# Kernel tuning notes

Measured on AMD Instinct MI355X. Metric: run time of the kernel, lower is better.

The kernel has to match this reference:

```python
import jax, jax.numpy as jnp
import numpy as np

N, E, F, DIM, BT, RANK = 8192, 32768, 16, 64, 4, 512
EDGE_VARIABLE = 2


def setup_inputs() -> dict:
    key = jax.random.key(0)
    ks = jax.random.split(key, 24)

    def rn(i, shape, s=0.05):
        return jax.random.normal(ks[i], shape, dtype=jnp.float32) * s

    x = jax.random.normal(ks[0], (N, F), dtype=jnp.float32)
    # first feature column is a categorical node-type id (EDGE_VARIABLE == 2)
    x = x.at[:, 0].set(jax.random.randint(ks[1], (N,), 0, 5).astype(jnp.float32))
    edge_index = jax.random.randint(ks[2], (2, E), 0, N, dtype=jnp.int32)
    edge_attr = jax.random.uniform(ks[3], (E, BT), dtype=jnp.float32)
    return {
        'x': x, 'edge_index': edge_index, 'edge_attr': edge_attr,
        'W0': rn(4, (DIM, F)), 'b0': jnp.zeros(DIM, jnp.float32),
        'nnW1': rn(5, (32, BT)), 'nnb1': jnp.zeros(32, jnp.float32),
        'nnW2': rn(6, (DIM * DIM, 32), 0.02), 'nnb2': jnp.zeros(DIM * DIM, jnp.float32),
        'root': rn(7, (DIM, DIM)), 'conv_b': jnp.zeros(DIM, jnp.float32),
        'Wih': rn(8, (3 * DIM, DIM)), 'Whh': rn(9, (3 * DIM, DIM)),
        'bih': jnp.zeros(3 * DIM, jnp.float32), 'bhh': jnp.zeros(3 * DIM, jnp.float32),
        'W1l': rn(10, (BT, DIM)), 'b1l': jnp.zeros(BT, jnp.float32),
        'WUp': rn(11, (DIM, BT)), 'bUp': jnp.zeros(DIM, jnp.float32),
        'WDown': rn(12, (BT, DIM)), 'bDown': jnp.zeros(BT, jnp.float32),
        'U': rn(13, (BT, RANK, DIM)), 'V': rn(14, (BT, DIM, RANK)),
        'weight': rn(15, (1, DIM), 1.0), 'linW': rn(16, (DIM, DIM)), 'linb': jnp.zeros(DIM, jnp.float32),
        'weight_e': rn(17, (1, BT), 1.0), 'linWe': rn(18, (BT, BT)), 'linbe': jnp.zeros(BT, jnp.float32),
    }


def _gru_cell(m, h, Wih, Whh, bih, bhh):
    # torch GRU gate order: reset, update, new
    gi = m @ Wih.T + bih
    gh = h @ Whh.T + bhh
    ir, iz, i_n = jnp.split(gi, 3, axis=-1)
    hr, hz, h_n = jnp.split(gh, 3, axis=-1)
    r = jax.nn.sigmoid(ir + hr)
    z = jax.nn.sigmoid(iz + hz)
    n = jnp.tanh(i_n + r * h_n)
    return (1.0 - z) * n + z * h


def reference(x, edge_index, edge_attr,
              W0, b0, nnW1, nnb1, nnW2, nnb2, root, conv_b,
              Wih, Whh, bih, bhh, W1l, b1l, WUp, bUp, WDown, bDown,
              U, V, weight, linW, linb, weight_e, linWe, linbe):
    n_nodes = x.shape[0]
    src, dst = edge_index[0], edge_index[1]

    out = jax.nn.relu(x @ W0.T + b0)            # [N, DIM]
    h = out

    # mean-aggregation degree (clamped)
    deg = jnp.clip(jax.ops.segment_sum(jnp.ones_like(src, dtype=out.dtype), dst,
                                       num_segments=n_nodes), 1.0)[:, None]

    # edge-conditioned per-edge weight matrices  [E, DIM, DIM]
    We = (jax.nn.relu(edge_attr @ nnW1.T + nnb1) @ nnW2.T + nnb2).reshape(-1, DIM, DIM)

    for _ in range(3):  # 3 message-passing + GRU steps
        msg = jnp.einsum('ei,eio->eo', out[src], We)                 # per-edge matvec
        agg = jax.ops.segment_sum(msg, dst, num_segments=n_nodes) / deg
        m = jax.nn.relu(out @ root + agg + conv_b)                    # NNConv(root + mean msg)
        h = _gru_cell(m, h, Wih, Whh, bih, bhh)
        out = h

    out_edges = jax.nn.relu(out @ W1l.T + b1l)                        # [N, BT]

    # combine node state with upscaled edge-variable state
    ev_mask = (x[:, 0] == EDGE_VARIABLE)
    out_combine = jnp.where(ev_mask[:, None], out_edges @ WUp.T + bUp, out)

    # FGNet factorized (rank-512) bond-type-conditioned message passing
    bond = jnp.argmax(edge_attr, axis=-1)                             # [E]
    oh = jax.nn.one_hot(bond, BT, dtype=out.dtype)                    # [E, BT]
    h_src = out_combine[src]                                          # [E, DIM]
    zf = jnp.einsum('ed,tdr->etr', h_src, V)                          # [E, BT, RANK]
    zsel = jnp.einsum('etr,et->er', zf, oh)                           # select factor by bond type
    me = jnp.einsum('er,et,trd->ed', zsel, oh, U)                     # [E, DIM]
    msg_f = jax.nn.relu(jax.ops.segment_sum(me, dst, num_segments=n_nodes) / deg)
    msg_to_edge = msg_f @ WDown.T + bDown                             # [N, BT]

    out = out + jax.nn.relu((weight * msg_f) @ linW.T + linb)
    out_edges = out_edges + jax.nn.relu((weight_e * msg_to_edge) @ linWe.T + linbe)
    return jax.nn.log_softmax(out_edges, axis=-1)
```

## Files before the change

### kernel.cpp

```cpp
#include <hip/hip_runtime.h>
#include <hip/hip_bf16.h>

#define NN 8192
#define NE 32768
#define FD 16
#define DIM 64
#define BT 4
#define RANK 512

typedef __attribute__((ext_vector_type(8))) short bf16x8;
typedef __attribute__((ext_vector_type(4))) float f32x4;

__device__ inline unsigned short f2bf(float f) {
    union { float f; unsigned u; } c; c.f = f;
    return (unsigned short)((c.u + 0x7fffu + ((c.u >> 16) & 1u)) >> 16);
}
__device__ inline float ubf(unsigned short h) {
    union { unsigned u; float f; } c; c.u = ((unsigned)h) << 16; return c.f;
}
__device__ inline float bflo(unsigned u) { union { unsigned u; float f; } c; c.u = u << 16; return c.f; }
__device__ inline float bfhi(unsigned u) { union { unsigned u; float f; } c; c.u = u & 0xffff0000u; return c.f; }

__global__ __launch_bounds__(256) void k_prep(
    const float* __restrict__ x, const int* __restrict__ ei, const float* __restrict__ ea,
    const float* __restrict__ W0, const float* __restrict__ b0,
    const float* __restrict__ nnW1, const float* __restrict__ nnb1,
    const float* __restrict__ W2, const float* __restrict__ Wih, const float* __restrict__ Whh,
    const float* __restrict__ root, const float* __restrict__ b2,
    const float* __restrict__ U, const float* __restrict__ V,
    float* __restrict__ s, unsigned short* __restrict__ shi, unsigned short* __restrict__ slo,
    float* __restrict__ deg, int* __restrict__ srccnt,
    float* __restrict__ h32, int* __restrict__ bond,
    unsigned short* __restrict__ w2h, unsigned short* __restrict__ w2l,
    unsigned short* __restrict__ wihh, unsigned short* __restrict__ wihl,
    unsigned short* __restrict__ whhh, unsigned short* __restrict__ whhl,
    unsigned short* __restrict__ rth, unsigned short* __restrict__ rtl,
    unsigned short* __restrict__ b2th, unsigned short* __restrict__ b2tl,
    float* __restrict__ M)
{
    int bid = blockIdx.x, tid = threadIdx.x;
    if (bid < 2048) {
        int gid = bid * 256 + tid;
        int n = gid >> 6, d = gid & 63;
        const float4* xr = (const float4*)(x + (size_t)n * FD);
        const float4* wr = (const float4*)(W0 + d * FD);
        float4 x0 = xr[0], x1 = xr[1], x2 = xr[2], x3 = xr[3];
        float4 w0 = wr[0], w1 = wr[1], w2 = wr[2], w3 = wr[3];
        float acc = b0[d]
            + x0.x*w0.x + x0.y*w0.y + x0.z*w0.z + x0.w*w0.w
            + x1.x*w1.x + x1.y*w1.y + x1.z*w1.z + x1.w*w1.w
            + x2.x*w2.x + x2.y*w2.y + x2.z*w2.z + x2.w*w2.w
            + x3.x*w3.x + x3.y*w3.y + x3.z*w3.z + x3.w*w3.w;
        float sv = fmaxf(acc, 0.f);
        s[gid] = sv;
        unsigned short h = f2bf(sv);
        shi[gid] = h; slo[gid] = f2bf(sv - ubf(h));
    } else if (bid < 2176) {
        int e = (bid - 2048) * 256 + tid;
        atomicAdd(&deg[ei[NE + e]], 1.0f);
        atomicAdd(&srccnt[ei[e]], 1);
    } else if (bid < 6272) {
        int e = (bid - 2176) * 8 + (tid >> 5);
        int k = tid & 31;
        float a0 = ea[e * 4 + 0], a1 = ea[e * 4 + 1], a2 = ea[e * 4 + 2], a3 = ea[e * 4 + 3];
        float h = nnb1[k] + a0 * nnW1[k * 4 + 0] + a1 * nnW1[k * 4 + 1]
                          + a2 * nnW1[k * 4 + 2] + a3 * nnW1[k * 4 + 3];
        h32[e * 32 + k] = fmaxf(h, 0.f);
        if (k == 0) {
            int bi = 0; float bv = a0;
            if (a1 > bv) { bv = a1; bi = 1; }
            if (a2 > bv) { bv = a2; bi = 2; }
            if (a3 > bv) { bv = a3; bi = 3; }
            bond[e] = bi;
        }
    } else if (bid < 6784) {
        int gid = (bid - 6272) * 256 + tid;
        int col = gid >> 6, i = gid & 63;
        float v = W2[(size_t)(i * 64 + (col >> 5)) * 32 + (col & 31)];
        unsigned short h = f2bf(v);
        w2h[gid] = h; w2l[gid] = f2bf(v - ubf(h));
    } else if (bid < 6880) {
        int gid = (bid - 6784) * 256 + tid;
        if (gid < 12288) {
            float v = Wih[gid];
            unsigned short h = f2bf(v);
            wihh[gid] = h; wihl[gid] = f2bf(v - ubf(h));
        } else {
            int g = gid - 12288;
            float v = Whh[g];
            unsigned short h = f2bf(v);
            whhh[g] = h; whhl[g] = f2bf(v - ubf(h));
        }
    } else if (bid < 6896) {
        int gid = (bid - 6880) * 256 + tid;
        int o = gid >> 6, i = gid & 63;
        float v = root[i * 64 + o];
        unsigned short h = f2bf(v);
        rth[gid] = h; rtl[gid] = f2bf(v - ubf(h));
    } else if (bid < 6912) {
        int gid = (bid - 6896) * 256 + tid;
        int o = gid >> 6, i = gid & 63;
        float v = b2[i * 64 + o];
        unsigned short h = f2bf(v);
        b2th[gid] = h; b2tl[gid] = f2bf(v - ubf(h));
    } else {
        __shared__ float red[4][64];
        int t = bid - 6912;
        int b = t >> 6, d = t & 63;
        int chunk = tid >> 6, dp = tid & 63;
        const float* Vp = V + ((size_t)b * DIM + d) * RANK;
        const float* Up = U + (size_t)b * RANK * DIM;
        float acc = 0.f;
        for (int r = chunk * 128; r < chunk * 128 + 128; ++r)
            acc += Vp[r] * Up[(size_t)r * DIM + dp];
        red[chunk][dp] = acc;
        __syncthreads();
        if (chunk == 0)
            M[((size_t)b * DIM + d) * DIM + dp] =
                red[0][dp] + red[1][dp] + red[2][dp] + red[3][dp];
    }
}

__global__ __launch_bounds__(1024) void k_scan(const int* __restrict__ cnt,
                                               int* __restrict__ start, int* __restrict__ cursor) {
    __shared__ int ls[1024];
    int tid = threadIdx.x;
    int v[8], tot = 0;
#pragma unroll
    for (int j = 0; j < 8; ++j) { v[j] = cnt[tid * 8 + j]; tot += v[j]; }
    ls[tid] = tot;
    __syncthreads();
    for (int off = 1; off < 1024; off <<= 1) {
        int t = (tid >= off) ? ls[tid - off] : 0;
        __syncthreads();
        ls[tid] += t;
        __syncthreads();
    }
    int run = ls[tid] - tot;
#pragma unroll
    for (int j = 0; j < 8; ++j) {
        start[tid * 8 + j] = run; cursor[tid * 8 + j] = run; run += v[j];
    }
}

__global__ __launch_bounds__(256) void k_scatter(const int* __restrict__ ei,
                                                 int* __restrict__ cursor, int* __restrict__ eord) {
    int e = blockIdx.x * 256 + threadIdx.x;
    int pos = atomicAdd(&cursor[ei[e]], 1);
    eord[pos] = e;
}

__global__ __launch_bounds__(256) void k_gemm_A(const unsigned short* __restrict__ sh,
                                                const unsigned short* __restrict__ sl,
                                                const unsigned short* __restrict__ wh,
                                                const unsigned short* __restrict__ wl,
                                                const unsigned short* __restrict__ b2th,
                                                const unsigned short* __restrict__ b2tl,
                                                unsigned short* __restrict__ A,
                                                float* __restrict__ cbuf) {
    int tid = threadIdx.x, wid = tid >> 6, lane = tid & 63;
    int lr = lane & 15, kg = lane >> 4;
    int m0 = blockIdx.x * 64;
    if (blockIdx.y == 8) {
        f32x4 acc[4] = {};
#pragma unroll
        for (int kb = 0; kb < 64; kb += 32) {
            size_t offA = (size_t)(m0 + wid * 16 + lr) * 64 + kb + kg * 8;
            bf16x8 ah = *(const bf16x8*)(sh + offA);
            bf16x8 al = *(const bf16x8*)(sl + offA);
#pragma unroll
            for (int ni = 0; ni < 4; ++ni) {
                size_t offB = (size_t)(ni * 16 + lr) * 64 + kb + kg * 8;
                bf16x8 bh = *(const bf16x8*)(b2th + offB);
                bf16x8 bl = *(const bf16x8*)(b2tl + offB);
                acc[ni] = __builtin_amdgcn_mfma_f32_16x16x32_bf16(ah, bh, acc[ni], 0, 0, 0);
                acc[ni] = __builtin_amdgcn_mfma_f32_16x16x32_bf16(ah, bl, acc[ni], 0, 0, 0);
                acc[ni] = __builtin_amdgcn_mfma_f32_16x16x32_bf16(al, bh, acc[ni], 0, 0, 0);
            }
        }
#pragma unroll
        for (int ni = 0; ni < 4; ++ni)
#pragma unroll
            for (int r = 0; r < 4; ++r)
                cbuf[(size_t)(m0 + wid * 16 + kg * 4 + r) * 64 + ni * 16 + lr] = acc[ni][r];
        return;
    }
    int n0 = blockIdx.y * 256 + wid * 64;
    f32x4 acc[4][4] = {};
#pragma unroll
    for (int kb = 0; kb < 64; kb += 32) {
        bf16x8 ah[4], al[4], bh[4], bl[4];
#pragma unroll
        for (int mi = 0; mi < 4; ++mi) {
            size_t off = (size_t)(m0 + mi * 16 + lr) * 64 + kb + kg * 8;
            ah[mi] = *(const bf16x8*)(sh + off);
            al[mi] = *(const bf16x8*)(sl + off);
        }
#pragma unroll
        for (int ni = 0; ni < 4; ++ni) {
            size_t off = (size_t)(n0 + ni * 16 + lr) * 64 + kb + kg * 8;
            bh[ni] = *(const bf16x8*)(wh + off);
            bl[ni] = *(const bf16x8*)(wl + off);
        }
#pragma unroll
        for (int mi = 0; mi < 4; ++mi)
#pragma unroll
            for (int ni = 0; ni < 4; ++ni) {
                acc[mi][ni] = __builtin_amdgcn_mfma_f32_16x16x32_bf16(ah[mi], bh[ni], acc[mi][ni], 0, 0, 0);
                acc[mi][ni] = __builtin_amdgcn_mfma_f32_16x16x32_bf16(ah[mi], bl[ni], acc[mi][ni], 0, 0, 0);
                acc[mi][ni] = __builtin_amdgcn_mfma_f32_16x16x32_bf16(al[mi], bh[ni], acc[mi][ni], 0, 0, 0);
            }
    }
#pragma unroll
    for (int mi = 0; mi < 4; ++mi)
#pragma unroll
        for (int r = 0; r < 4; ++r) {
            size_t row = (size_t)(m0 + mi * 16 + kg * 4 + r) * 2048;
#pragma unroll
            for (int ni = 0; ni < 4; ++ni)
                A[row + n0 + ni * 16 + lr] = f2bf(acc[mi][ni][r]);
        }
}

__global__ __launch_bounds__(256) void k_edge(const int* __restrict__ ei,
                                              const int* __restrict__ start,
                                              const int* __restrict__ srccnt,
                                              const int* __restrict__ eord,
                                              const float* __restrict__ h32,
                                              const unsigned short* __restrict__ A,
                                              const float* __restrict__ cbuf,
                                              float* __restrict__ agg) {
    int tid = threadIdx.x, wid = tid >> 6, o = tid & 63;
    int n = blockIdx.x * 4 + wid;
    int cnt = srccnt[n];
    if (cnt == 0) return;
    int beg = start[n];
    float cv = cbuf[(size_t)n * DIM + o];
    const uint4* Ap = (const uint4*)(A + (size_t)n * 2048 + o * 32);
    uint4 a0 = Ap[0], a1 = Ap[1], a2 = Ap[2], a3 = Ap[3];
    for (int i = beg; i < beg + cnt; ++i) {
        int e = eord[i];
        int dst = ei[NE + e];
        const float4* hp = (const float4*)(h32 + (size_t)e * 32);
        float acc = cv;
        float4 hA = hp[0], hB = hp[1];
        acc += hA.x*bflo(a0.x) + hA.y*bfhi(a0.x) + hA.z*bflo(a0.y) + hA.w*bfhi(a0.y)
             + hB.x*bflo(a0.z) + hB.y*bfhi(a0.z) + hB.z*bflo(a0.w) + hB.w*bfhi(a0.w);
        hA = hp[2]; hB = hp[3];
        acc += hA.x*bflo(a1.x) + hA.y*bfhi(a1.x) + hA.z*bflo(a1.y) + hA.w*bfhi(a1.y)
             + hB.x*bflo(a1.z) + hB.y*bfhi(a1.z) + hB.z*bflo(a1.w) + hB.w*bfhi(a1.w);
        hA = hp[4]; hB = hp[5];
        acc += hA.x*bflo(a2.x) + hA.y*bfhi(a2.x) + hA.z*bflo(a2.y) + hA.w*bfhi(a2.y)
             + hB.x*bflo(a2.z) + hB.y*bfhi(a2.z) + hB.z*bflo(a2.w) + hB.w*bfhi(a2.w);
        hA = hp[6]; hB = hp[7];
        acc += hA.x*bflo(a3.x) + hA.y*bfhi(a3.x) + hA.z*bflo(a3.y) + hA.w*bfhi(a3.y)
             + hB.x*bflo(a3.z) + hB.y*bfhi(a3.z) + hB.z*bflo(a3.w) + hB.w*bfhi(a3.w);
        atomicAdd(&agg[(size_t)dst * DIM + o], acc);
    }
}

__global__ __launch_bounds__(64) void k_upd(
    float* __restrict__ s, unsigned short* __restrict__ shi, unsigned short* __restrict__ slo,
    float* __restrict__ agg, const float* __restrict__ deg, const float* __restrict__ conv_b,
    const unsigned short* __restrict__ rth, const unsigned short* __restrict__ rtl,
    const unsigned short* __restrict__ wihh, const unsigned short* __restrict__ wihl,
    const unsigned short* __restrict__ whhh, const unsigned short* __restrict__ whhl,
    const float* __restrict__ bih, const float* __restrict__ bhh)
{
    __shared__ unsigned short mh_l[16 * 64];
    __shared__ unsigned short ml_l[16 * 64];
    int lane = threadIdx.x;
    int lr = lane & 15, kg = lane >> 4;
    int m0 = blockIdx.x * 16;

    bf16x8 sa_h[2], sa_l[2];
#pragma unroll
    for (int kb = 0; kb < 2; ++kb) {
        size_t off = (size_t)(m0 + lr) * 64 + kb * 32 + kg * 8;
        sa_h[kb] = *(const bf16x8*)(shi + off);
        sa_l[kb] = *(const bf16x8*)(slo + off);
    }
    f32x4 macc[4] = {};
#pragma unroll
    for (int kb = 0; kb < 2; ++kb)
#pragma unroll
        for (int ni = 0; ni < 4; ++ni) {
            size_t offB = (size_t)(ni * 16 + lr) * 64 + kb * 32 + kg * 8;
            bf16x8 bh = *(const bf16x8*)(rth + offB);
            bf16x8 bl = *(const bf16x8*)(rtl + offB);
            macc[ni] = __builtin_amdgcn_mfma_f32_16x16x32_bf16(sa_h[kb], bh, macc[ni], 0, 0, 0);
            macc[ni] = __builtin_amdgcn_mfma_f32_16x16x32_bf16(sa_h[kb], bl, macc[ni], 0, 0, 0);
            macc[ni] = __builtin_amdgcn_mfma_f32_16x16x32_bf16(sa_l[kb], bh, macc[ni], 0, 0, 0);
        }
#pragma unroll
    for (int r = 0; r < 4; ++r) {
        int row = m0 + kg * 4 + r;
        float inv = 1.f / fmaxf(deg[row], 1.f);
#pragma unroll
        for (int ni = 0; ni < 4; ++ni) {
            int col = ni * 16 + lr;
            size_t idx = (size_t)row * 64 + col;
            float v = macc[ni][r] + agg[idx] * inv + conv_b[col];
            agg[idx] = 0.f;
            v = fmaxf(v, 0.f);
            unsigned short h = f2bf(v);
            int loff = (kg * 4 + r) * 64 + col;
            mh_l[loff] = h; ml_l[loff] = f2bf(v - ubf(h));
        }
    }
    __syncthreads();
    bf16x8 ma_h[2], ma_l[2];
#pragma unroll
    for (int kb = 0; kb < 2; ++kb) {
        int loff = lr * 64 + kb * 32 + kg * 8;
        ma_h[kb] = *(const bf16x8*)(mh_l + loff);
        ma_l[kb] = *(const bf16x8*)(ml_l + loff);
    }
    f32x4 gacc[12] = {}, hacc[12] = {};
#pragma unroll
    for (int kb = 0; kb < 2; ++kb)
#pragma unroll
        for (int ni = 0; ni < 12; ++ni) {
            size_t offB = (size_t)(ni * 16 + lr) * 64 + kb * 32 + kg * 8;
            bf16x8 bh = *(const bf16x8*)(wihh + offB);
            bf16x8 bl = *(const bf16x8*)(wihl + offB);
            gacc[ni] = __builtin_amdgcn_mfma_f32_16x16x32_bf16(ma_h[kb], bh, gacc[ni], 0, 0, 0);
            gacc[ni] = __builtin_amdgcn_mfma_f32_16x16x32_bf16(ma_h[kb], bl, gacc[ni], 0, 0, 0);
            gacc[ni] = __builtin_amdgcn_mfma_f32_16x16x32_bf16(ma_l[kb], bh, gacc[ni], 0, 0, 0);
            bf16x8 ch = *(const bf16x8*)(whhh + offB);
            bf16x8 cl = *(const bf16x8*)(whhl + offB);
            hacc[ni] = __builtin_amdgcn_mfma_f32_16x16x32_bf16(sa_h[kb], ch, hacc[ni], 0, 0, 0);
            hacc[ni] = __builtin_amdgcn_mfma_f32_16x16x32_bf16(sa_h[kb], cl, hacc[ni], 0, 0, 0);
            hacc[ni] = __builtin_amdgcn_mfma_f32_16x16x32_bf16(sa_l[kb], ch, hacc[ni], 0, 0, 0);
        }
#pragma unroll
    for (int j = 0; j < 4; ++j) {
        int d = lr + 16 * j;
        float bi0 = bih[d], bi1 = bih[64 + d], bi2 = bih[128 + d];
        float bh0 = bhh[d], bh1 = bhh[64 + d], bh2 = bhh[128 + d];
#pragma unroll
        for (int r = 0; r < 4; ++r) {
            int row = m0 + kg * 4 + r;
            size_t idx = (size_t)row * 64 + d;
            float ir = gacc[j][r], iz = gacc[4 + j][r], in_ = gacc[8 + j][r];
            float hr_ = hacc[j][r], hz = hacc[4 + j][r], hn = hacc[8 + j][r];
            float hv = s[idx];
            float rg = 1.f / (1.f + expf(-(ir + bi0 + hr_ + bh0)));
            float z  = 1.f / (1.f + expf(-(iz + bi1 + hz + bh1)));
            float nv = tanhf(in_ + bi2 + rg * (hn + bh2));
            float nh = (1.f - z) * nv + z * hv;
            s[idx] = nh;
            unsigned short hb = f2bf(nh);
            shi[idx] = hb; slo[idx] = f2bf(nh - ubf(hb));
        }
    }
}

__global__ __launch_bounds__(256) void k_edges_out(const float* __restrict__ s,
                                                   const float* __restrict__ x,
                                                   const float* __restrict__ W1l,
                                                   const float* __restrict__ b1l,
                                                   const float* __restrict__ WUp,
                                                   const float* __restrict__ bUp,
                                                   float* __restrict__ oe,
                                                   float* __restrict__ oc) {
    __shared__ float sm_s[4][64];
    __shared__ float sm_oe[4][4];
    int tid = threadIdx.x, w = tid >> 6, lane = tid & 63;
    int node = blockIdx.x * 4 + w;
    float sv = s[(size_t)node * DIM + lane];
    sm_s[w][lane] = sv;
    __syncthreads();
    if (lane < 4) {
        float acc = b1l[lane];
        for (int i = 0; i < 64; ++i) acc += sm_s[w][i] * W1l[lane * 64 + i];
        acc = fmaxf(acc, 0.f);
        sm_oe[w][lane] = acc;
        oe[(size_t)node * 4 + lane] = acc;
    }
    __syncthreads();
    float ocv;
    if (x[(size_t)node * FD] == 2.0f) {
        ocv = bUp[lane];
#pragma unroll
        for (int t = 0; t < 4; ++t) ocv += sm_oe[w][t] * WUp[lane * 4 + t];
    } else {
        ocv = sv;
    }
    oc[(size_t)node * DIM + lane] = ocv;
}

__global__ __launch_bounds__(256) void k_fgedge(const int* __restrict__ ei,
                                                const int* __restrict__ bond,
                                                const float* __restrict__ oc,
                                                const float* __restrict__ M,
                                                float* __restrict__ fg_agg) {
    __shared__ float so[4][64];
    int tid = threadIdx.x, w = tid >> 6, lane = tid & 63;
    int e = blockIdx.x * 4 + w;
    int src = ei[e], dst = ei[NE + e];
    int b = bond[e];
    so[w][lane] = oc[(size_t)src * DIM + lane];
    __syncthreads();
    float acc = 0.f;
    const float* Mp = M + b * DIM * DIM;
    for (int d = 0; d < 64; ++d) acc += so[w][d] * Mp[d * 64 + lane];
    atomicAdd(&fg_agg[(size_t)dst * DIM + lane], acc);
}

__global__ __launch_bounds__(256) void k_final(const float* __restrict__ fg_agg,
                                               const float* __restrict__ deg,
                                               const float* __restrict__ oe,
                                               const float* __restrict__ WDown,
                                               const float* __restrict__ bDown,
                                               const float* __restrict__ weight_e,
                                               const float* __restrict__ linWe,
                                               const float* __restrict__ linbe,
                                               float* __restrict__ out) {
    int tid = threadIdx.x, w = tid >> 6, lane = tid & 63;
    int node = blockIdx.x * 4 + w;
    float degc = fmaxf(deg[node], 1.f);
    float mf = fmaxf(fg_agg[(size_t)node * DIM + lane] / degc, 0.f);
    float mte[4];
#pragma unroll
    for (int t = 0; t < 4; ++t) {
        float p = mf * WDown[t * 64 + lane];
#pragma unroll
        for (int off = 32; off; off >>= 1) p += __shfl_xor(p, off);
        mte[t] = p + bDown[t];
    }
    float val[4];
    float mx = -1e30f;
#pragma unroll
    for (int t = 0; t < 4; ++t) {
        float acc = linbe[t];
#pragma unroll
        for (int t2 = 0; t2 < 4; ++t2) acc += weight_e[t2] * mte[t2] * linWe[t * 4 + t2];
        val[t] = oe[(size_t)node * 4 + t] + fmaxf(acc, 0.f);
        mx = fmaxf(mx, val[t]);
    }
    float lse = 0.f;
#pragma unroll
    for (int t = 0; t < 4; ++t) lse += expf(val[t] - mx);
    lse = logf(lse);
    if (lane < 4) out[(size_t)node * 4 + lane] = val[lane] - mx - lse;
}

extern "C" void kernel_launch(void* const* d_in, const int* in_sizes, int n_in,
                              void* d_out, int out_size, void* d_ws, size_t ws_size,
                              hipStream_t stream) {
    const float* x       = (const float*)d_in[0];
    const int*   ei      = (const int*)  d_in[1];
    const float* ea      = (const float*)d_in[2];
    const float* W0      = (const float*)d_in[3];
    const float* b0      = (const float*)d_in[4];
    const float* nnW1    = (const float*)d_in[5];
    const float* nnb1    = (const float*)d_in[6];
    const float* nnW2    = (const float*)d_in[7];
    const float* nnb2    = (const float*)d_in[8];
    const float* root    = (const float*)d_in[9];
    const float* conv_b  = (const float*)d_in[10];
    const float* Wih     = (const float*)d_in[11];
    const float* Whh     = (const float*)d_in[12];
    const float* bih     = (const float*)d_in[13];
    const float* bhh     = (const float*)d_in[14];
    const float* W1l     = (const float*)d_in[15];
    const float* b1l     = (const float*)d_in[16];
    const float* WUp     = (const float*)d_in[17];
    const float* bUp     = (const float*)d_in[18];
    const float* WDown   = (const float*)d_in[19];
    const float* bDown   = (const float*)d_in[20];
    const float* U       = (const float*)d_in[21];
    const float* V       = (const float*)d_in[22];
    const float* weight_e= (const float*)d_in[26];
    const float* linWe   = (const float*)d_in[27];
    const float* linbe   = (const float*)d_in[28];
    float* out = (float*)d_out;

    char* ws = (char*)d_ws;
    size_t off = 0;
    auto alloc = [&](size_t bytes) { size_t o = off; off = (off + bytes + 255) & ~(size_t)255; return o; };
    float* deg    = (float*)(ws + alloc((size_t)NN * 4));
    int*   srccnt = (int*)  (ws + alloc((size_t)NN * 4));
    float* agg    = (float*)(ws + alloc((size_t)NN * DIM * 4));
    float* fg_agg = (float*)(ws + alloc((size_t)NN * DIM * 4));
    float* s      = (float*)(ws + alloc((size_t)NN * DIM * 4));
    unsigned short* shi = (unsigned short*)(ws + alloc((size_t)NN * DIM * 2));
    unsigned short* slo = (unsigned short*)(ws + alloc((size_t)NN * DIM * 2));
    float* cbuf   = (float*)(ws + alloc((size_t)NN * DIM * 4));
    float* h32    = (float*)(ws + alloc((size_t)NE * 32 * 4));
    int*   bond   = (int*)  (ws + alloc((size_t)NE * 4));
    int*   startp = (int*)  (ws + alloc((size_t)NN * 4));
    int*   cursor = (int*)  (ws + alloc((size_t)NN * 4));
    int*   eord   = (int*)  (ws + alloc((size_t)NE * 4));
    float* oe     = (float*)(ws + alloc((size_t)NN * 4 * 4));
    float* oc     = (float*)(ws + alloc((size_t)NN * DIM * 4));
    float* Mbuf   = (float*)(ws + alloc((size_t)BT * DIM * DIM * 4));
    unsigned short* w2h = (unsigned short*)(ws + alloc((size_t)2048 * 64 * 2));
    unsigned short* w2l = (unsigned short*)(ws + alloc((size_t)2048 * 64 * 2));
    unsigned short* wihh = (unsigned short*)(ws + alloc((size_t)192 * 64 * 2));
    unsigned short* wihl = (unsigned short*)(ws + alloc((size_t)192 * 64 * 2));
    unsigned short* whhh = (unsigned short*)(ws + alloc((size_t)192 * 64 * 2));
    unsigned short* whhl = (unsigned short*)(ws + alloc((size_t)192 * 64 * 2));
    unsigned short* rth  = (unsigned short*)(ws + alloc((size_t)64 * 64 * 2));
    unsigned short* rtl  = (unsigned short*)(ws + alloc((size_t)64 * 64 * 2));
    unsigned short* b2th = (unsigned short*)(ws + alloc((size_t)64 * 64 * 2));
    unsigned short* b2tl = (unsigned short*)(ws + alloc((size_t)64 * 64 * 2));
    unsigned short* Abuf = (unsigned short*)(ws + alloc((size_t)NN * 2048 * 2));
    (void)n_in; (void)in_sizes; (void)out_size; (void)ws_size;

    hipMemsetAsync(deg, 0, (size_t)2 * NN * 4, stream);
    hipMemsetAsync(agg, 0, (size_t)2 * NN * DIM * 4, stream);

    k_prep<<<7168, 256, 0, stream>>>(x, ei, ea, W0, b0, nnW1, nnb1,
                                     nnW2, Wih, Whh, root, nnb2, U, V,
                                     s, shi, slo, deg, srccnt, h32, bond,
                                     w2h, w2l, wihh, wihl, whhh, whhl,
                                     rth, rtl, b2th, b2tl, Mbuf);
    k_scan<<<1, 1024, 0, stream>>>(srccnt, startp, cursor);
    k_scatter<<<NE / 256, 256, 0, stream>>>(ei, cursor, eord);

    for (int it = 0; it < 3; ++it) {
        k_gemm_A<<<dim3(NN / 64, 9), 256, 0, stream>>>(shi, slo, w2h, w2l, b2th, b2tl,
                                                       Abuf, cbuf);
        k_edge<<<NN / 4, 256, 0, stream>>>(ei, startp, srccnt, eord, h32, Abuf, cbuf, agg);
        k_upd<<<NN / 16, 64, 0, stream>>>(s, shi, slo, agg, deg, conv_b,
                                          rth, rtl, wihh, wihl, whhh, whhl, bih, bhh);
    }

    k_edges_out<<<NN / 4, 256, 0, stream>>>(s, x, W1l, b1l, WUp, bUp, oe, oc);
    k_fgedge<<<NE / 4, 256, 0, stream>>>(ei, bond, oc, Mbuf, fg_agg);
    k_final<<<NN / 4, 256, 0, stream>>>(fg_agg, deg, oe, WDown, bDown, weight_e, linWe, linbe, out);
}
```

Measured before the change: 269.1 us.

## Split GRU update kernel across four waves per 16-row tile

The k_upd kernel now runs 256 threads (four wavefronts) per 16-node tile instead of one. Each wave computes a 16-column slice of the root matmul and three of the twelve gate tiles. Gate pre-activations are exchanged through a 24KB shared-memory buffer before the elementwise GRU step. This is meant to cut the long serial MFMA chain and register pressure per wave and raise parallelism, at the cost of an extra barrier and more LDS per block.

Measured after the change: 242.1 us. -10.0%, faster.

```diff
diff --git a/kernel.cpp b/kernel.cpp
--- a/kernel.cpp
+++ b/kernel.cpp
@@ -259,7 +259,7 @@
     }
 }
 
-__global__ __launch_bounds__(64) void k_upd(
+__global__ __launch_bounds__(256) void k_upd(
     float* __restrict__ s, unsigned short* __restrict__ shi, unsigned short* __restrict__ slo,
     float* __restrict__ agg, const float* __restrict__ deg, const float* __restrict__ conv_b,
     const unsigned short* __restrict__ rth, const unsigned short* __restrict__ rtl,
@@ -269,7 +269,9 @@
 {
     __shared__ unsigned short mh_l[16 * 64];
     __shared__ unsigned short ml_l[16 * 64];
-    int lane = threadIdx.x;
+    __shared__ float gl[16 * 384];
+    int tid = threadIdx.x;
+    int wid = tid >> 6, lane = tid & 63;
     int lr = lane & 15, kg = lane >> 4;
     int m0 = blockIdx.x * 16;
 
@@ -280,35 +282,32 @@
         sa_h[kb] = *(const bf16x8*)(shi + off);
         sa_l[kb] = *(const bf16x8*)(slo + off);
     }
-    f32x4 macc[4] = {};
-#pragma unroll
-    for (int kb = 0; kb < 2; ++kb)
-#pragma unroll
-        for (int ni = 0; ni < 4; ++ni) {
-            size_t offB = (size_t)(ni * 16 + lr) * 64 + kb * 32 + kg * 8;
-            bf16x8 bh = *(const bf16x8*)(rth + offB);
-            bf16x8 bl = *(const bf16x8*)(rtl + offB);
-            macc[ni] = __builtin_amdgcn_mfma_f32_16x16x32_bf16(sa_h[kb], bh, macc[ni], 0, 0, 0);
-            macc[ni] = __builtin_amdgcn_mfma_f32_16x16x32_bf16(sa_h[kb], bl, macc[ni], 0, 0, 0);
-            macc[ni] = __builtin_amdgcn_mfma_f32_16x16x32_bf16(sa_l[kb], bh, macc[ni], 0, 0, 0);
-        }
+
+    f32x4 macc = {};
+#pragma unroll
+    for (int kb = 0; kb < 2; ++kb) {
+        size_t offB = (size_t)(wid * 16 + lr) * 64 + kb * 32 + kg * 8;
+        bf16x8 bh = *(const bf16x8*)(rth + offB);
+        bf16x8 bl = *(const bf16x8*)(rtl + offB);
+        macc = __builtin_amdgcn_mfma_f32_16x16x32_bf16(sa_h[kb], bh, macc, 0, 0, 0);
+        macc = __builtin_amdgcn_mfma_f32_16x16x32_bf16(sa_h[kb], bl, macc, 0, 0, 0);
+        macc = __builtin_amdgcn_mfma_f32_16x16x32_bf16(sa_l[kb], bh, macc, 0, 0, 0);
+    }
 #pragma unroll
     for (int r = 0; r < 4; ++r) {
         int row = m0 + kg * 4 + r;
         float inv = 1.f / fmaxf(deg[row], 1.f);
-#pragma unroll
-        for (int ni = 0; ni < 4; ++ni) {
-            int col = ni * 16 + lr;
-            size_t idx = (size_t)row * 64 + col;
-            float v = macc[ni][r] + agg[idx] * inv + conv_b[col];
-            agg[idx] = 0.f;
-            v = fmaxf(v, 0.f);
-            unsigned short h = f2bf(v);
-            int loff = (kg * 4 + r) * 64 + col;
-            mh_l[loff] = h; ml_l[loff] = f2bf(v - ubf(h));
-        }
+        int col = wid * 16 + lr;
+        size_t idx = (size_t)row * 64 + col;
+        float v = macc[r] + agg[idx] * inv + conv_b[col];
+        agg[idx] = 0.f;
+        v = fmaxf(v, 0.f);
+        unsigned short h = f2bf(v);
+        int loff = (kg * 4 + r) * 64 + col;
+        mh_l[loff] = h; ml_l[loff] = f2bf(v - ubf(h));
     }
     __syncthreads();
+
     bf16x8 ma_h[2], ma_l[2];
 #pragma unroll
     for (int kb = 0; kb < 2; ++kb) {
@@ -316,43 +315,51 @@
         ma_h[kb] = *(const bf16x8*)(mh_l + loff);
         ma_l[kb] = *(const bf16x8*)(ml_l + loff);
     }
-    f32x4 gacc[12] = {}, hacc[12] = {};
+    f32x4 gacc[3] = {}, hacc[3] = {};
 #pragma unroll
     for (int kb = 0; kb < 2; ++kb)
 #pragma unroll
-        for (int ni = 0; ni < 12; ++ni) {
+        for (int j = 0; j < 3; ++j) {
+            int ni = wid * 3 + j;
             size_t offB = (size_t)(ni * 16 + lr) * 64 + kb * 32 + kg * 8;
             bf16x8 bh = *(const bf16x8*)(wihh + offB);
             bf16x8 bl = *(const bf16x8*)(wihl + offB);
-            gacc[ni] = __builtin_amdgcn_mfma_f32_16x16x32_bf16(ma_h[kb], bh, gacc[ni], 0, 0, 0);
-            gacc[ni] = __builtin_amdgcn_mfma_f32_16x16x32_bf16(ma_h[kb], bl, gacc[ni], 0, 0, 0);
-            gacc[ni] = __builtin_amdgcn_mfma_f32_16x16x32_bf16(ma_l[kb], bh, gacc[ni], 0, 0, 0);
+            gacc[j] = __builtin_amdgcn_mfma_f32_16x16x32_bf16(ma_h[kb], bh, gacc[j], 0, 0, 0);
+            gacc[j] = __builtin_amdgcn_mfma_f32_16x16x32_bf16(ma_h[kb], bl, gacc[j], 0, 0, 0);
+            gacc[j] = __builtin_amdgcn_mfma_f32_16x16x32_bf16(ma_l[kb], bh, gacc[j], 0, 0, 0);
             bf16x8 ch = *(const bf16x8*)(whhh + offB);
             bf16x8 cl = *(const bf16x8*)(whhl + offB);
-            hacc[ni] = __builtin_amdgcn_mfma_f32_16x16x32_bf16(sa_h[kb], ch, hacc[ni], 0, 0, 0);
-            hacc[ni] = __builtin_amdgcn_mfma_f32_16x16x32_bf16(sa_h[kb], cl, hacc[ni], 0, 0, 0);
-            hacc[ni] = __builtin_amdgcn_mfma_f32_16x16x32_bf16(sa_l[kb], ch, hacc[ni], 0, 0, 0);
-        }
-#pragma unroll
-    for (int j = 0; j < 4; ++j) {
-        int d = lr + 16 * j;
-        float bi0 = bih[d], bi1 = bih[64 + d], bi2 = bih[128 + d];
-        float bh0 = bhh[d], bh1 = bhh[64 + d], bh2 = bhh[128 + d];
+            hacc[j] = __builtin_amdgcn_mfma_f32_16x16x32_bf16(sa_h[kb], ch, hacc[j], 0, 0, 0);
+            hacc[j] = __builtin_amdgcn_mfma_f32_16x16x32_bf16(sa_h[kb], cl, hacc[j], 0, 0, 0);
+            hacc[j] = __builtin_amdgcn_mfma_f32_16x16x32_bf16(sa_l[kb], ch, hacc[j], 0, 0, 0);
+        }
+#pragma unroll
+    for (int j = 0; j < 3; ++j)
 #pragma unroll
         for (int r = 0; r < 4; ++r) {
-            int row = m0 + kg * 4 + r;
-            size_t idx = (size_t)row * 64 + d;
-            float ir = gacc[j][r], iz = gacc[4 + j][r], in_ = gacc[8 + j][r];
-            float hr_ = hacc[j][r], hz = hacc[4 + j][r], hn = hacc[8 + j][r];
-            float hv = s[idx];
-            float rg = 1.f / (1.f + expf(-(ir + bi0 + hr_ + bh0)));
-            float z  = 1.f / (1.f + expf(-(iz + bi1 + hz + bh1)));
-            float nv = tanhf(in_ + bi2 + rg * (hn + bh2));
-            float nh = (1.f - z) * nv + z * hv;
-            s[idx] = nh;
-            unsigned short hb = f2bf(nh);
-            shi[idx] = hb; slo[idx] = f2bf(nh - ubf(hb));
-        }
+            int row = kg * 4 + r;
+            int col = (wid * 3 + j) * 16 + lr;
+            gl[row * 384 + col] = gacc[j][r];
+            gl[row * 384 + 192 + col] = hacc[j][r];
+        }
+    __syncthreads();
+
+#pragma unroll
+    for (int k = 0; k < 4; ++k) {
+        int item = tid + k * 256;
+        int row = item >> 6, d = item & 63;
+        size_t idx = (size_t)(m0 + row) * 64 + d;
+        const float* gr = gl + row * 384;
+        float ir = gr[d], iz = gr[64 + d], in_ = gr[128 + d];
+        float hr_ = gr[192 + d], hz = gr[256 + d], hn = gr[320 + d];
+        float hv = s[idx];
+        float rg = 1.f / (1.f + expf(-(ir + bih[d] + hr_ + bhh[d])));
+        float z  = 1.f / (1.f + expf(-(iz + bih[64 + d] + hz + bhh[64 + d])));
+        float nv = tanhf(in_ + bih[128 + d] + rg * (hn + bhh[128 + d]));
+        float nh = (1.f - z) * nv + z * hv;
+        s[idx] = nh;
+        unsigned short hb = f2bf(nh);
+        shi[idx] = hb; slo[idx] = f2bf(nh - ubf(hb));
     }
 }
 
@@ -524,8 +531,8 @@
         k_gemm_A<<<dim3(NN / 64, 9), 256, 0, stream>>>(shi, slo, w2h, w2l, b2th, b2tl,
                                                        Abuf, cbuf);
         k_edge<<<NN / 4, 256, 0, stream>>>(ei, startp, srccnt, eord, h32, Abuf, cbuf, agg);
-        k_upd<<<NN / 16, 64, 0, stream>>>(s, shi, slo, agg, deg, conv_b,
-                                          rth, rtl, wihh, wihl, whhh, whhl, bih, bhh);
+        k_upd<<<NN / 16, 256, 0, stream>>>(s, shi, slo, agg, deg, conv_b,
+                                           rth, rtl, wihh, wihl, whhh, whhl, bih, bhh);
     }
 
     k_edges_out<<<NN / 4, 256, 0, stream>>>(s, x, W1l, b1l, WUp, bUp, oe, oc);
```
